# Kernel optimization log

Measured on AMD Instinct MI355X. Metric: run time of the kernel, lower is better.

## Reference

```python
import jax, jax.numpy as jnp
import numpy as np

EPS = 1e-7
NUM_HEADS = 16

def _ln(x, g, b):
    m = jnp.mean(x, -1, keepdims=True)
    v = jnp.var(x, -1, keepdims=True)
    return (x - m) * jax.lax.rsqrt(v + EPS) * g + b

def _gelu(x):
    return jax.nn.gelu(x, approximate=False)  # torch nn.GELU default = exact erf

def _attn(x, qkv_w, qkv_b, pw, pb):
    B, N, C = x.shape
    D = C // NUM_HEADS
    qkv = (x @ qkv_w.T + qkv_b).reshape(B, N, 3, NUM_HEADS, D).transpose(2, 0, 3, 1, 4)
    q, k, v = qkv[0], qkv[1], qkv[2]
    a = jax.nn.softmax(jnp.einsum('bhnd,bhmd->bhnm', q, k) * (D ** -0.5), axis=-1)
    o = jnp.einsum('bhnm,bhmd->bhnd', a, v).transpose(0, 2, 1, 3).reshape(B, N, C)
    return o @ pw.T + pb

def _gcn(x, w, b, adj):
    # x: (B,C,J); w: (C*K,C) 1x1 conv, then einsum 'nkctv,kvw->nctw' with t==1
    K = adj.shape[0]
    B, C, J = x.shape
    y = jnp.einsum('bcj,oc->boj', x, w) + b[None, :, None]
    y = y.reshape(B, K, C, J)
    return jnp.einsum('bkcv,kvw->bcw', y, adj)

def _mlp(x, w1, b1, w2, b2):
    return _gelu(_gelu(x @ w1.T + b1) @ w2.T + b2)

def _lrsc(x, adj, l1g, l1b, l2g, l2b, g1w, g1b, g2w, g2b, m1w, m1b, m2w, m2b):
    x = x.transpose(0, 2, 1)                       # (B,C,J)
    res = x
    xn = _ln(x, l1g, l1b)                          # LayerNorm over J
    x = res + _mlp(xn, m1w, m1b, m2w, m2b) + _gcn(xn, g1w, g1b, adj)
    x = _ln(x.transpose(0, 2, 1), l2g, l2b).transpose(0, 2, 1)  # LayerNorm over C
    res = x
    x = res + _mlp(x, m1w, m1b, m2w, m2b) + _gcn(x, g2w, g2b, adj)
    return x.transpose(0, 2, 1)                    # (B,J,C)

def _gkpc(x, lg, lb, q1w, q1b, p1w, p1b, q2w, q2b, p2w, p2b):
    x = x + _attn(_ln(x, lg, lb), q1w, q1b, p1w, p1b)
    return _attn(_ln(x, lg, lb), q2w, q2b, p2w, p2b)  # note: no residual on second attn

def _forward(x, adj, ln1_g, ln1_b, ln2_g, ln2_b, gcn1_w, gcn1_b, gcn2_w, gcn2_b,
             mlp1_w1, mlp1_b1, mlp1_w2, mlp1_b2, attn_ln_g, attn_ln_b,
             qkv1_w, qkv1_b, proj1_w, proj1_b, qkv2_w, qkv2_b, proj2_w, proj2_b,
             tn_g, tn_b):
    L = ln1_g.shape[0]
    for i in range(L):
        # GG_ACM/RR_ACM/LCM are published as identity -> both 0.3/0.7 mixes equal x + gelu(x)
        xin = x + _gelu(x)
        x5 = _gkpc(xin, attn_ln_g[i], attn_ln_b[i], qkv1_w[i], qkv1_b[i],
                   proj1_w[i], proj1_b[i], qkv2_w[i], qkv2_b[i], proj2_w[i], proj2_b[i])
        x7 = _lrsc(xin, adj, ln1_g[i], ln1_b[i], ln2_g[i], ln2_b[i],
                   gcn1_w[i], gcn1_b[i], gcn2_w[i], gcn2_b[i],
                   mlp1_w1[i], mlp1_b1[i], mlp1_w2[i], mlp1_b2[i])
        x = x + x5 + x7
    return _ln(x, tn_g, tn_b)

def setup_inputs():
    B, V, C, K, L = 2048, 17, 512, 3, 3
    s = 0.05
    ks = jax.random.split(jax.random.key(0), 12)
    rn = lambda k, sh: jax.random.normal(k, sh, jnp.float32) * s
    return dict(
        x=jax.random.normal(ks[0], (B, V, C), jnp.float32),
        adj=jax.random.uniform(ks[1], (K, V, V), dtype=jnp.float32),
        ln1_g=jnp.ones((L, V), jnp.float32), ln1_b=jnp.zeros((L, V), jnp.float32),
        ln2_g=jnp.ones((L, C), jnp.float32), ln2_b=jnp.zeros((L, C), jnp.float32),
        gcn1_w=rn(ks[2], (L, C * K, C)), gcn1_b=jnp.zeros((L, C * K), jnp.float32),
        gcn2_w=rn(ks[3], (L, C * K, C)), gcn2_b=jnp.zeros((L, C * K), jnp.float32),
        mlp1_w1=rn(ks[4], (L, C, V)), mlp1_b1=jnp.zeros((L, C), jnp.float32),
        mlp1_w2=rn(ks[5], (L, V, C)), mlp1_b2=jnp.zeros((L, V), jnp.float32),
        attn_ln_g=jnp.ones((L, C), jnp.float32), attn_ln_b=jnp.zeros((L, C), jnp.float32),
        qkv1_w=rn(ks[6], (L, 3 * C, C)), qkv1_b=jnp.zeros((L, 3 * C), jnp.float32),
        proj1_w=rn(ks[7], (L, C, C)), proj1_b=jnp.zeros((L, C), jnp.float32),
        qkv2_w=rn(ks[8], (L, 3 * C, C)), qkv2_b=jnp.zeros((L, 3 * C), jnp.float32),
        proj2_w=rn(ks[9], (L, C, C)), proj2_b=jnp.zeros((L, C), jnp.float32),
        tn_g=jnp.ones((C,), jnp.float32), tn_b=jnp.zeros((C,), jnp.float32),
    )

def reference(x, adj, ln1_g, ln1_b, ln2_g, ln2_b, gcn1_w, gcn1_b, gcn2_w, gcn2_b,
              mlp1_w1, mlp1_b1, mlp1_w2, mlp1_b2, attn_ln_g, attn_ln_b,
              qkv1_w, qkv1_b, proj1_w, proj1_b, qkv2_w, qkv2_b, proj2_w, proj2_b,
              tn_g, tn_b):
    return _forward(x, adj, ln1_g, ln1_b, ln2_g, ln2_b, gcn1_w, gcn1_b, gcn2_w, gcn2_b,
                    mlp1_w1, mlp1_b1, mlp1_w2, mlp1_b2, attn_ln_g, attn_ln_b,
                    qkv1_w, qkv1_b, proj1_w, proj1_b, qkv2_w, qkv2_b, proj2_w, proj2_b,
                    tn_g, tn_b)
```

## Files before the change

kernel.cpp:

```cpp
#include <hip/hip_runtime.h>
#include <hip/hip_bf16.h>
#include <math.h>

#define Bn 2048
#define Vn 17
#define Cn 512
static const size_t NE = (size_t)Bn * Vn * Cn;
#define MROWS (Bn * Vn)

typedef __attribute__((ext_vector_type(8))) short bf16x8;
typedef __attribute__((ext_vector_type(4))) float f32x4;
typedef __attribute__((ext_vector_type(2))) float f32x2;
typedef unsigned short u16;

__device__ __forceinline__ float u2f(u16 u) { return __uint_as_float(((unsigned)u) << 16); }
__device__ __forceinline__ u16 f2u(float f) {
    unsigned u = __float_as_uint(f);
    return (u16)((u + 0x7fffu + ((u >> 16) & 1u)) >> 16);
}
__device__ __forceinline__ float gelu_f(float x) {
    return 0.5f * x * (1.0f + erff(x * 0.70710678118654752f));
}
__device__ __forceinline__ float exp2f_fast(float b) {
#if __has_builtin(__builtin_amdgcn_exp2f)
    return __builtin_amdgcn_exp2f(b);
#else
    return __expf(b * 0.69314718056f);
#endif
}
__device__ __forceinline__ float gelu_fast(float x) {
    float b = x * fmaf(x * x, -0.10294348f, -2.30220820f);
    return x * __builtin_amdgcn_rcpf(1.0f + exp2f_fast(b));
}
__device__ __forceinline__ unsigned pk2(float lo, float hi) {
    __hip_bfloat162 h = __float22bfloat162_rn(make_float2(lo, hi));
    unsigned r;
    __builtin_memcpy(&r, &h, 4);
    return r;
}
__device__ __forceinline__ unsigned gelu2pk(float x0, float x1) {
    f32x2 x = {x0, x1};
    f32x2 xx = x * x;
    f32x2 t = xx * (f32x2){-0.10294348f, -0.10294348f} +
              (f32x2){-2.30220820f, -2.30220820f};
    f32x2 b = x * t;
    f32x2 e = {exp2f_fast(b[0]), exp2f_fast(b[1])};
    f32x2 d = e + (f32x2){1.0f, 1.0f};
    f32x2 r = {__builtin_amdgcn_rcpf(d[0]), __builtin_amdgcn_rcpf(d[1])};
    f32x2 g = x * r;
    return pk2(g[0], g[1]);
}
__device__ __forceinline__ void gload16(const u16* g, u16* l) {
    __builtin_amdgcn_global_load_lds((const __attribute__((address_space(1))) void*)g,
                                     (__attribute__((address_space(3))) void*)l, 16, 0, 0);
}

__global__ void k_diag(float* __restrict__ o, float v, int n) {
    int i = blockIdx.x * 256 + threadIdx.x;
    if (i < n) o[i] = v;
}

__global__ void k_f2b(const float4* __restrict__ s, ushort4* __restrict__ d, int n4) {
    int i = blockIdx.x * 256 + threadIdx.x;
    if (i >= n4) return;
    float4 v = s[i];
    ushort4 o = {f2u(v.x), f2u(v.y), f2u(v.z), f2u(v.w)};
    d[i] = o;
}

__global__ void k_mpad(const float* __restrict__ W1, const float* __restrict__ W2,
                       u16* __restrict__ W1p, u16* __restrict__ W2p) {
    int t = blockIdx.x * 256 + threadIdx.x;
    if (t < 512 * 32) {
        int o = t >> 5, j = t & 31;
        W1p[t] = (j < 17) ? f2u(W1[o * 17 + j]) : (u16)0;
    } else {
        int t2 = t - 512 * 32;
        int w = t2 >> 9;
        W2p[t2] = (w < 17) ? f2u(W2[t2]) : (u16)0;
    }
}

__global__ __launch_bounds__(256) void k_xin_lnc(const float* __restrict__ X,
                                                 const float* __restrict__ g,
                                                 const float* __restrict__ bt,
                                                 u16* __restrict__ XIN, u16* __restrict__ T,
                                                 int nrows) {
    int row = blockIdx.x * 4 + (threadIdx.x >> 6);
    if (row >= nrows) return;
    int lane = threadIdx.x & 63;
    const float* xp = X + (size_t)row * Cn + lane * 8;
    float4 v0 = *(const float4*)xp, v1 = *(const float4*)(xp + 4);
    float xv[8] = {v0.x, v0.y, v0.z, v0.w, v1.x, v1.y, v1.z, v1.w};
    bf16x8 xr;
    float vv[8];
#pragma unroll
    for (int k = 0; k < 8; k++) {
        u16 h = f2u(xv[k] + gelu_f(xv[k]));
        xr[k] = (short)h;
        vv[k] = u2f(h);
    }
    *(bf16x8*)(XIN + (size_t)row * Cn + lane * 8) = xr;
    float s = 0.f, q = 0.f;
#pragma unroll
    for (int k = 0; k < 8; k++) { s += vv[k]; q = fmaf(vv[k], vv[k], q); }
#pragma unroll
    for (int o = 32; o; o >>= 1) { s += __shfl_xor(s, o); q += __shfl_xor(q, o); }
    float mean = s * (1.f / Cn);
    float var = q * (1.f / Cn) - mean * mean;
    float inv = 1.f / sqrtf(var + 1e-7f);
    int cb = lane * 8;
    bf16x8 r;
#pragma unroll
    for (int k = 0; k < 8; k++) r[k] = f2u((vv[k] - mean) * inv * g[cb + k] + bt[cb + k]);
    *(bf16x8*)(T + (size_t)row * Cn + cb) = r;
}

template <int F32IO>
__global__ __launch_bounds__(256) void k_ln_c(const void* __restrict__ Xv,
                                              const float* __restrict__ g,
                                              const float* __restrict__ bt,
                                              void* __restrict__ Ov, int nrows) {
    int row = blockIdx.x * 4 + (threadIdx.x >> 6);
    if (row >= nrows) return;
    int lane = threadIdx.x & 63;
    float vv[8];
    if (F32IO) {
        const float* xp = (const float*)Xv + (size_t)row * Cn + lane * 8;
        float4 v0 = *(const float4*)xp, v1 = *(const float4*)(xp + 4);
        vv[0] = v0.x; vv[1] = v0.y; vv[2] = v0.z; vv[3] = v0.w;
        vv[4] = v1.x; vv[5] = v1.y; vv[6] = v1.z; vv[7] = v1.w;
    } else {
        bf16x8 h = *(const bf16x8*)((const u16*)Xv + (size_t)row * Cn + lane * 8);
#pragma unroll
        for (int k = 0; k < 8; k++) vv[k] = u2f((u16)h[k]);
    }
    float s = 0.f, q = 0.f;
#pragma unroll
    for (int k = 0; k < 8; k++) { s += vv[k]; q = fmaf(vv[k], vv[k], q); }
#pragma unroll
    for (int o = 32; o; o >>= 1) { s += __shfl_xor(s, o); q += __shfl_xor(q, o); }
    float mean = s * (1.f / Cn);
    float var = q * (1.f / Cn) - mean * mean;
    float inv = 1.f / sqrtf(var + 1e-7f);
    int cb = lane * 8;
    if (F32IO) {
        float r[8];
#pragma unroll
        for (int k = 0; k < 8; k++) r[k] = (vv[k] - mean) * inv * g[cb + k] + bt[cb + k];
        float* op = (float*)Ov + (size_t)row * Cn + cb;
        *(float4*)op = make_float4(r[0], r[1], r[2], r[3]);
        *(float4*)(op + 4) = make_float4(r[4], r[5], r[6], r[7]);
    } else {
        bf16x8 r;
#pragma unroll
        for (int k = 0; k < 8; k++) r[k] = f2u((vv[k] - mean) * inv * g[cb + k] + bt[cb + k]);
        *(bf16x8*)((u16*)Ov + (size_t)row * Cn + cb) = r;
    }
}

__global__ __launch_bounds__(256) void k_ln_j(const u16* __restrict__ X,
                                              const float* __restrict__ g,
                                              const float* __restrict__ bt,
                                              u16* __restrict__ O) {
    int idx = blockIdx.x * 256 + threadIdx.x;
    int b = idx >> 9, c = idx & 511;
    const u16* xp = X + (size_t)b * Vn * Cn + c;
    float v[Vn];
    float s = 0.f;
#pragma unroll
    for (int j = 0; j < Vn; j++) { v[j] = u2f(xp[(size_t)j * Cn]); s += v[j]; }
    float mean = s * (1.f / Vn);
    float q = 0.f;
#pragma unroll
    for (int j = 0; j < Vn; j++) { float d = v[j] - mean; q = fmaf(d, d, q); }
    float inv = 1.f / sqrtf(q * (1.f / Vn) + 1e-7f);
    u16* op = O + (size_t)b * Vn * Cn + c;
#pragma unroll
    for (int j = 0; j < Vn; j++) op[(size_t)j * Cn] = f2u((v[j] - mean) * inv * g[j] + bt[j]);
}

template <int REMAP, int EPI>
__global__ __launch_bounds__(256) void k_gemm(const u16* __restrict__ A, const u16* __restrict__ W,
                                              const float* __restrict__ bias, u16* __restrict__ OutB,
                                              const u16* __restrict__ Res, float* __restrict__ Xf,
                                              int hbase, int shift) {
    constexpr int NT = REMAP ? 6 : 8;
    const int K = 512;
    int wave = threadIdx.x >> 6, lane = threadIdx.x & 63;
    int m0 = blockIdx.x * 128 + wave * 32;
    int nbase = blockIdx.y * (16 * NT);
    int r16 = lane & 15, kq = lane >> 4;
    int ld = REMAP ? (3 << shift) : 512;

    const u16* wp[NT];
    int wrow[NT];
#pragma unroll
    for (int nt = 0; nt < NT; nt++) {
        int n = nbase + nt * 16 + r16;
        int wr;
        if (REMAP) {
            int s = n >> shift, off = n & ((1 << shift) - 1);
            wr = (s << 9) + hbase + off;
        } else wr = n;
        wrow[nt] = wr;
        wp[nt] = W + (size_t)wr * K + kq * 8;
    }
    f32x4 acc[2][NT];
#pragma unroll
    for (int i = 0; i < 2; i++)
#pragma unroll
        for (int nt = 0; nt < NT; nt++) acc[i][nt] = (f32x4){0.f, 0.f, 0.f, 0.f};

    const u16* ap = A + (size_t)(m0 + r16) * K + kq * 8;
    for (int k0 = 0; k0 < K; k0 += 32) {
        bf16x8 a0 = *(const bf16x8*)(ap + k0);
        bf16x8 a1 = *(const bf16x8*)(ap + (size_t)16 * K + k0);
#pragma unroll
        for (int nt = 0; nt < NT; nt++) {
            bf16x8 bf = *(const bf16x8*)(wp[nt] + k0);
            acc[0][nt] = __builtin_amdgcn_mfma_f32_16x16x32_bf16(a0, bf, acc[0][nt], 0, 0, 0);
            acc[1][nt] = __builtin_amdgcn_mfma_f32_16x16x32_bf16(a1, bf, acc[1][nt], 0, 0, 0);
        }
    }
#pragma unroll
    for (int nt = 0; nt < NT; nt++) {
        float bv = bias[wrow[nt]];
        int n = nbase + nt * 16 + r16;
#pragma unroll
        for (int i = 0; i < 2; i++) {
#pragma unroll
            for (int r = 0; r < 4; r++) {
                size_t mb = (size_t)(m0 + i * 16 + kq * 4 + r);
                float v = acc[i][nt][r] + bv;
                if (EPI == 0) OutB[mb * ld + n] = f2u(v);
                else if (EPI == 1) { size_t o = mb * 512 + n; OutB[o] = f2u(v + u2f(Res[o])); }
                else { size_t o = mb * 512 + n; Xf[o] += v; }
            }
        }
    }
}

template <int EPI, int NY>
__global__ __launch_bounds__(256) void k_gemm2(const u16* __restrict__ A, const u16* __restrict__ W,
                                               const float* __restrict__ bias, u16* __restrict__ OutB,
                                               const u16* __restrict__ Res, float* __restrict__ Xf,
                                               int N) {
    __shared__ u16 As[128 * 64];
    __shared__ u16 Bs[128 * 64];
    const int K = 512;
    int tid = threadIdx.x;
    int wave = tid >> 6, lane = tid & 63;
    int cpx = gridDim.x >> 3;
    int bid = blockIdx.x;
    int swz = (bid & 7) * cpx + (bid >> 3);
    int m0 = (swz / NY) * 128, n0 = (swz % NY) * 128;
    int r16 = lane & 15, kq = lane >> 4;

    int srow = wave << 2;
    int lrow = lane >> 3;
    int lcol = (lane & 7) * 8;

    f32x4 acc[2][8];
#pragma unroll
    for (int i = 0; i < 2; i++)
#pragma unroll
        for (int j = 0; j < 8; j++) acc[i][j] = (f32x4){0.f, 0.f, 0.f, 0.f};

    const u16* aT = As + (wave * 32 + r16) * 64 + kq * 8;
    const u16* bT = Bs + r16 * 64 + kq * 8;

    for (int k0 = 0; k0 < K; k0 += 64) {
#pragma unroll
        for (int i = 0; i < 4; i++) {
            int rows = (srow + i) * 8 + lrow;
            gload16(A + (size_t)(m0 + rows) * K + k0 + lcol, (u16*)As + (srow + i) * 512);
            gload16(W + (size_t)(n0 + rows) * K + k0 + lcol, (u16*)Bs + (srow + i) * 512);
        }
        __syncthreads();
#pragma unroll
        for (int kk = 0; kk < 64; kk += 32) {
            bf16x8 af0 = *(const bf16x8*)(aT + kk);
            bf16x8 af1 = *(const bf16x8*)(aT + 16 * 64 + kk);
#pragma unroll
            for (int nt = 0; nt < 8; nt++) {
                bf16x8 bf = *(const bf16x8*)(bT + nt * 16 * 64 + kk);
                acc[0][nt] = __builtin_amdgcn_mfma_f32_16x16x32_bf16(af0, bf, acc[0][nt], 0, 0, 0);
                acc[1][nt] = __builtin_amdgcn_mfma_f32_16x16x32_bf16(af1, bf, acc[1][nt], 0, 0, 0);
            }
        }
        __syncthreads();
    }

    int mw = m0 + wave * 32;
#pragma unroll
    for (int nt = 0; nt < 8; nt++) {
        int n = n0 + nt * 16 + r16;
        float bv = bias[n];
#pragma unroll
        for (int i = 0; i < 2; i++) {
#pragma unroll
            for (int r = 0; r < 4; r++) {
                size_t mb = (size_t)(mw + i * 16 + kq * 4 + r);
                size_t o = mb * N + n;
                float v = acc[i][nt][r] + bv;
                if (EPI == 0) OutB[o] = f2u(v);
                else if (EPI == 1) OutB[o] = f2u(v + u2f(Res[o]));
                else Xf[o] += v;
            }
        }
    }
}

__global__ __launch_bounds__(256) void k_attn(const u16* __restrict__ Y, u16* __restrict__ T,
                                              int shift, int hgbase, int l2ch) {
    int wv = threadIdx.x >> 6, lane = threadIdx.x & 63;
    if (lane >= 34) return;
    int gw = blockIdx.x * 4 + wv;
    int which = (lane >= 17) ? 1 : 0;
    int j = lane - which * 17;
    int pid = gw * 2 + which;
    int b = pid >> l2ch;
    int hl = pid & ((1 << l2ch) - 1);
    int CW = 1 << shift;
    int row3 = 3 << shift;

    const u16* qb = Y + (size_t)(b * Vn + j) * row3 + hl * 32;
    float q[32];
#pragma unroll
    for (int d0 = 0; d0 < 32; d0 += 8) {
        bf16x8 h = *(const bf16x8*)(qb + d0);
#pragma unroll
        for (int d = 0; d < 8; d++) q[d0 + d] = u2f((u16)h[d]);
    }
    float sc[Vn];
    float mx = -1e30f;
#pragma unroll
    for (int kk = 0; kk < Vn; kk++) {
        const u16* kb = Y + (size_t)(b * Vn + kk) * row3 + CW + hl * 32;
        float s = 0.f;
#pragma unroll
        for (int d0 = 0; d0 < 32; d0 += 8) {
            bf16x8 h = *(const bf16x8*)(kb + d0);
#pragma unroll
            for (int d = 0; d < 8; d++) s = fmaf(q[d0 + d], u2f((u16)h[d]), s);
        }
        s *= 0.1767766952966369f;
        sc[kk] = s;
        mx = fmaxf(mx, s);
    }
    float sum = 0.f;
#pragma unroll
    for (int kk = 0; kk < Vn; kk++) { sc[kk] = __expf(sc[kk] - mx); sum += sc[kk]; }
    float inv = 1.f / sum;
    float o[32];
#pragma unroll
    for (int d = 0; d < 32; d++) o[d] = 0.f;
#pragma unroll
    for (int kk = 0; kk < Vn; kk++) {
        const u16* vb = Y + (size_t)(b * Vn + kk) * row3 + 2 * CW + hl * 32;
        float p = sc[kk] * inv;
#pragma unroll
        for (int d0 = 0; d0 < 32; d0 += 8) {
            bf16x8 h = *(const bf16x8*)(vb + d0);
#pragma unroll
            for (int d = 0; d < 8; d++) o[d0 + d] = fmaf(p, u2f((u16)h[d]), o[d0 + d]);
        }
    }
    u16* op = T + (size_t)(b * Vn + j) * Cn + hgbase + hl * 32;
#pragma unroll
    for (int d0 = 0; d0 < 32; d0 += 8) {
        bf16x8 r;
#pragma unroll
        for (int d = 0; d < 8; d++) r[d] = f2u(o[d0 + d]);
        *(bf16x8*)(op + d0) = r;
    }
}

template <int MODE>
__global__ __launch_bounds__(256) void k_agg(const u16* __restrict__ Y, const float* __restrict__ Adj,
                                             const u16* __restrict__ aux1, const u16* __restrict__ aux2,
                                             u16* __restrict__ OutB, float* __restrict__ Xf,
                                             int cbase, int shift) {
    __shared__ float adj_s[3][Vn][Vn];
    for (int t = threadIdx.x; t < 3 * Vn * Vn; t += 256) {
        int k = t / (Vn * Vn), r = t - k * Vn * Vn;
        adj_s[k][r / Vn][r % Vn] = Adj[t];
    }
    __syncthreads();
    int CW = 1 << shift;
    int idx = blockIdx.x * 256 + threadIdx.x;
    int b = idx >> shift, co = idx & (CW - 1);
    int c = cbase + co;
    int row3 = 3 << shift;
    float acc[Vn];
#pragma unroll
    for (int w = 0; w < Vn; w++) acc[w] = 0.f;
    const u16* yb = Y + (size_t)b * Vn * row3 + co;
#pragma unroll
    for (int k = 0; k < 3; k++)
#pragma unroll
        for (int v = 0; v < Vn; v++) {
            float y = u2f(yb[(size_t)v * row3 + k * CW]);
#pragma unroll
            for (int w = 0; w < Vn; w++) acc[w] = fmaf(y, adj_s[k][v][w], acc[w]);
        }
    size_t rb = (size_t)(b * Vn) * Cn + c;
#pragma unroll
    for (int w = 0; w < Vn; w++) {
        size_t o = rb + (size_t)w * Cn;
        float val = acc[w] + u2f(aux1[o]) + u2f(aux2[o]);
        if (MODE == 0) OutB[o] = f2u(val);
        else Xf[o] += val;
    }
}

__global__ __launch_bounds__(512) void k_mlp(const u16* __restrict__ X,
                                             const u16* __restrict__ W1p, const float* __restrict__ B1,
                                             const u16* __restrict__ W2p, const float* __restrict__ B2,
                                             u16* __restrict__ O) {
    __shared__ u16 Xs[256 * 40];
    __shared__ u16 Hs[256 * 40];
    int b = blockIdx.x >> 1;
    int cbase = (blockIdx.x & 1) << 8;
    int tid = threadIdx.x;

    for (int i = tid; i < 256 * 40 / 8; i += 512) ((float4*)Xs)[i] = make_float4(0.f, 0.f, 0.f, 0.f);
    __syncthreads();
    const u16* xb = X + (size_t)b * (Vn * Cn) + cbase;
    for (int i = tid; i < 17 * 256; i += 512) {
        int j = i >> 8, c = i & 255;
        Xs[c * 40 + j] = xb[j * Cn + c];
    }
    __syncthreads();

    int wave = tid >> 6, lane = tid & 63;
    int r16 = lane & 15, kq = lane >> 4;
    int crow = wave * 32;

    bf16x8 xf0 = *(const bf16x8*)(Xs + (crow + r16) * 40 + kq * 8);
    bf16x8 xf1 = *(const bf16x8*)(Xs + (crow + 16 + r16) * 40 + kq * 8);

    f32x4 acc2[2][2];
#pragma unroll
    for (int i = 0; i < 2; i++)
#pragma unroll
        for (int j = 0; j < 2; j++) acc2[i][j] = (f32x4){0.f, 0.f, 0.f, 0.f};

    const u16* hs0 = Hs + (crow + r16) * 40 + kq * 8;
    const u16* w1b = W1p + (r16 << 5) + kq * 8;
    const u16* w2b = W2p + (size_t)r16 * 512 + kq * 8;
    const u16* w2c = W2p + (size_t)16 * 512 + kq * 8;
    const float* b1b = B1 + kq * 4;

#pragma unroll
    for (int s = 0; s < 16; s++) {
        bf16x8 af0 = *(const bf16x8*)(w1b + s * 1024);
        bf16x8 af1 = *(const bf16x8*)(w1b + s * 1024 + 512);
        f32x4 bi0 = *(const f32x4*)(b1b + s * 32);
        f32x4 bi1 = *(const f32x4*)(b1b + s * 32 + 16);
        f32x4 a00 = __builtin_amdgcn_mfma_f32_16x16x32_bf16(af0, xf0, bi0, 0, 0, 0);
        f32x4 a01 = __builtin_amdgcn_mfma_f32_16x16x32_bf16(af0, xf1, bi0, 0, 0, 0);
        f32x4 a10 = __builtin_amdgcn_mfma_f32_16x16x32_bf16(af1, xf0, bi1, 0, 0, 0);
        f32x4 a11 = __builtin_amdgcn_mfma_f32_16x16x32_bf16(af1, xf1, bi1, 0, 0, 0);
#define STORE_H(ACC, NT, OT)                                                             \
        {                                                                                 \
            unsigned g0 = gelu2pk(ACC[0], ACC[1]);                                        \
            unsigned g1 = gelu2pk(ACC[2], ACC[3]);                                        \
            *(uint2*)(Hs + (crow + NT * 16 + r16) * 40 + OT * 16 + kq * 4) =              \
                make_uint2(g0, g1);                                                       \
        }
        STORE_H(a00, 0, 0)
        STORE_H(a01, 1, 0)
        STORE_H(a10, 0, 1)
        STORE_H(a11, 1, 1)
#undef STORE_H
        __builtin_amdgcn_sched_barrier(0);
        bf16x8 h0 = *(const bf16x8*)hs0;
        bf16x8 h1 = *(const bf16x8*)(hs0 + 16 * 40);
        bf16x8 wf0 = *(const bf16x8*)(w2b + s * 32);
        bf16x8 wf1 = *(const bf16x8*)(w2c + s * 32);
        acc2[0][0] = __builtin_amdgcn_mfma_f32_16x16x32_bf16(h0, wf0, acc2[0][0], 0, 0, 0);
        acc2[0][1] = __builtin_amdgcn_mfma_f32_16x16x32_bf16(h0, wf1, acc2[0][1], 0, 0, 0);
        acc2[1][0] = __builtin_amdgcn_mfma_f32_16x16x32_bf16(h1, wf0, acc2[1][0], 0, 0, 0);
        acc2[1][1] = __builtin_amdgcn_mfma_f32_16x16x32_bf16(h1, wf1, acc2[1][1], 0, 0, 0);
    }

    u16* ob = O + (size_t)b * (Vn * Cn) + cbase;
#pragma unroll
    for (int nt = 0; nt < 2; nt++) {
        int cl = crow + nt * 16 + kq * 4;
#pragma unroll
        for (int n2 = 0; n2 < 2; n2++) {
            int w = n2 * 16 + r16;
            if (w < 17) {
                float bb = B2[w];
                f32x4 v = acc2[nt][n2];
                uint2 pk = make_uint2(gelu2pk(v[0] + bb, v[1] + bb),
                                      gelu2pk(v[2] + bb, v[3] + bb));
                *(uint2*)(ob + (size_t)w * Cn + cl) = pk;
            }
        }
    }
}

extern "C" void kernel_launch(void* const* d_in, const int* in_sizes, int n_in,
                              void* d_out, int out_size, void* d_ws, size_t ws_size,
                              hipStream_t stream) {
    (void)in_sizes; (void)n_in; (void)out_size;
    typedef const float* fp;
    fp x_in = (fp)d_in[0];
    fp adj = (fp)d_in[1];
    fp ln1_g = (fp)d_in[2], ln1_b = (fp)d_in[3];
    fp ln2_g = (fp)d_in[4], ln2_b = (fp)d_in[5];
    fp gcn1_w = (fp)d_in[6], gcn1_b = (fp)d_in[7];
    fp gcn2_w = (fp)d_in[8], gcn2_b = (fp)d_in[9];
    fp m1w = (fp)d_in[10], m1b = (fp)d_in[11];
    fp m2w = (fp)d_in[12], m2b = (fp)d_in[13];
    fp aln_g = (fp)d_in[14], aln_b = (fp)d_in[15];
    fp qkv1_w = (fp)d_in[16], qkv1_b = (fp)d_in[17];
    fp p1w = (fp)d_in[18], p1b = (fp)d_in[19];
    fp qkv2_w = (fp)d_in[20], qkv2_b = (fp)d_in[21];
    fp p2w = (fp)d_in[22], p2b = (fp)d_in[23];
    fp tn_g = (fp)d_in[24], tn_b = (fp)d_in[25];

    const size_t NE2 = NE * 2;
    const size_t YCH16 = (size_t)MROWS * 96 * 16 * 2;
    const size_t SZ_QKV3 = (size_t)3 * 1536 * 512;
    const size_t SZ_P3 = (size_t)3 * 512 * 512;
    const size_t MPADL = (size_t)(512 * 32 + 32 * 512);
    const size_t POOLB = (4 * SZ_QKV3 + 2 * SZ_P3 + 3 * MPADL) * 2;
    const size_t WSCR_SZ = (size_t)1536 * 512 * 2;
    const size_t MPAD_SZ = MPADL * 2;

    bool FULLW = false;
    int CH = 0;
    if (3 * NE2 + YCH16 + POOLB + 1024 <= ws_size) { FULLW = true; CH = 16; }
    else {
        for (int ch = 16; ch >= 1; ch >>= 1) {
            size_t need = 3 * NE2 + WSCR_SZ + MPAD_SZ + (size_t)MROWS * 96 * ch * 2 + 1024;
            if (need <= ws_size) { CH = ch; break; }
        }
    }
    if (!CH) {
        k_diag<<<(int)((NE + 255) / 256), 256, 0, stream>>>((float*)d_out, (float)ws_size, (int)NE);
        return;
    }
    const int l2ch = __builtin_ctz(CH);
    const int shift = 5 + l2ch;
    const int NCH = 16 / CH;
    const bool FAST = (CH == 16);

    char* p = (char*)d_ws;
    u16* XIN = (u16*)p;  p += NE2;
    u16* T1 = (u16*)p;   p += NE2;
    u16* T2 = (u16*)p;   p += NE2;
    u16* YCH = (u16*)p;  p += (size_t)MROWS * 96 * CH * 2;
    u16 *WQ1 = nullptr, *WQ2 = nullptr, *WG1 = nullptr, *WG2 = nullptr,
        *WP1 = nullptr, *WP2 = nullptr, *MP1 = nullptr, *MP2 = nullptr, *WSCR = nullptr;
    if (FULLW) {
        WQ1 = (u16*)p; p += SZ_QKV3 * 2;
        WQ2 = (u16*)p; p += SZ_QKV3 * 2;
        WG1 = (u16*)p; p += SZ_QKV3 * 2;
        WG2 = (u16*)p; p += SZ_QKV3 * 2;
        WP1 = (u16*)p; p += SZ_P3 * 2;
        WP2 = (u16*)p; p += SZ_P3 * 2;
        MP1 = (u16*)p; p += 3 * 16384 * 2;
        MP2 = (u16*)p; p += 3 * 16384 * 2;
    } else {
        WSCR = (u16*)p; p += WSCR_SZ;
        MP1 = (u16*)p;  p += 16384 * 2;
        MP2 = (u16*)p;
    }

    float* X = (float*)d_out;
    (void)hipMemcpyAsync(X, x_in, NE * 4, hipMemcpyDeviceToDevice, stream);

    if (FULLW) {
        k_f2b<<<2304, 256, 0, stream>>>((const float4*)qkv1_w, (ushort4*)WQ1, (int)(SZ_QKV3 / 4));
        k_f2b<<<2304, 256, 0, stream>>>((const float4*)qkv2_w, (ushort4*)WQ2, (int)(SZ_QKV3 / 4));
        k_f2b<<<2304, 256, 0, stream>>>((const float4*)gcn1_w, (ushort4*)WG1, (int)(SZ_QKV3 / 4));
        k_f2b<<<2304, 256, 0, stream>>>((const float4*)gcn2_w, (ushort4*)WG2, (int)(SZ_QKV3 / 4));
        k_f2b<<<768, 256, 0, stream>>>((const float4*)p1w, (ushort4*)WP1, (int)(SZ_P3 / 4));
        k_f2b<<<768, 256, 0, stream>>>((const float4*)p2w, (ushort4*)WP2, (int)(SZ_P3 / 4));
        for (int l = 0; l < 3; l++)
            k_mpad<<<128, 256, 0, stream>>>(m1w + (size_t)l * Cn * Vn, m2w + (size_t)l * Vn * Cn,
                                            MP1 + l * 16384, MP2 + l * 16384);
    }

    const int GLN = MROWS / 4;
    const int GBC = Bn * Cn / 256;
    const int GATT = (Bn << l2ch) / 8;
    const int GAGG = (Bn << shift) / 256;
    const dim3 GEMM_C(MROWS / 128, CH);
    const dim3 GEMM_P(MROWS / 128, 4);
    const int CV_QKV = (int)(1536 * 512 / 4 / 256);
    const int CV_P = (int)(512 * 512 / 4 / 256);
    const int GQF = (MROWS / 128) * 12;
    const int GPF = (MROWS / 128) * 4;

    for (int i = 0; i < 3; i++) {
        fp q1w = qkv1_w + (size_t)i * 1536 * 512, q1b = qkv1_b + i * 1536;
        fp q2w = qkv2_w + (size_t)i * 1536 * 512, q2b = qkv2_b + i * 1536;
        fp g1w = gcn1_w + (size_t)i * 1536 * 512, g1b = gcn1_b + i * 1536;
        fp g2w = gcn2_w + (size_t)i * 1536 * 512, g2b = gcn2_b + i * 1536;
        fp pw1 = p1w + (size_t)i * 512 * 512, pb1 = p1b + i * Cn;
        fp pw2 = p2w + (size_t)i * 512 * 512, pb2 = p2b + i * Cn;
        fp alg = aln_g + i * Cn, alb = aln_b + i * Cn;
        fp l1g = ln1_g + i * Vn, l1b_ = ln1_b + i * Vn;
        fp l2g = ln2_g + i * Cn, l2b_ = ln2_b + i * Cn;
        fp w1 = m1w + (size_t)i * Cn * Vn, b1 = m1b + i * Cn;
        fp w2 = m2w + (size_t)i * Vn * Cn, b2 = m2b + i * Vn;

        const u16* wq1p = FULLW ? WQ1 + (size_t)i * 1536 * 512 : WSCR;
        const u16* wq2p = FULLW ? WQ2 + (size_t)i * 1536 * 512 : WSCR;
        const u16* wg1p = FULLW ? WG1 + (size_t)i * 1536 * 512 : WSCR;
        const u16* wg2p = FULLW ? WG2 + (size_t)i * 1536 * 512 : WSCR;
        const u16* wp1p = FULLW ? WP1 + (size_t)i * 512 * 512 : WSCR;
        const u16* wp2p = FULLW ? WP2 + (size_t)i * 512 * 512 : WSCR;
        const u16* mp1 = FULLW ? MP1 + i * 16384 : MP1;
        const u16* mp2 = FULLW ? MP2 + i * 16384 : MP2;

        if (!FULLW) k_mpad<<<128, 256, 0, stream>>>(w1, w2, (u16*)mp1, (u16*)mp2);

        k_xin_lnc<<<GLN, 256, 0, stream>>>(X, alg, alb, XIN, T1, MROWS);
        if (!FULLW) k_f2b<<<CV_QKV, 256, 0, stream>>>((const float4*)q1w, (ushort4*)WSCR, 1536 * 512 / 4);
        if (FAST) {
            k_gemm2<0, 12><<<GQF, 256, 0, stream>>>(T1, wq1p, q1b, YCH, nullptr, nullptr, 1536);
            k_attn<<<GATT, 256, 0, stream>>>(YCH, T2, shift, 0, l2ch);
        } else {
            for (int hg = 0; hg < NCH; hg++) {
                k_gemm<1, 0><<<GEMM_C, 256, 0, stream>>>(T1, WSCR, q1b, YCH, nullptr, nullptr, hg << shift, shift);
                k_attn<<<GATT, 256, 0, stream>>>(YCH, T2, shift, hg << shift, l2ch);
            }
        }
        if (!FULLW) k_f2b<<<CV_P, 256, 0, stream>>>((const float4*)pw1, (ushort4*)WSCR, 512 * 512 / 4);
        if (FAST) k_gemm2<1, 4><<<GPF, 256, 0, stream>>>(T2, wp1p, pb1, T1, XIN, nullptr, 512);
        else k_gemm<0, 1><<<GEMM_P, 256, 0, stream>>>(T2, WSCR, pb1, T1, XIN, nullptr, 0, 0);
        k_ln_c<0><<<GLN, 256, 0, stream>>>(T1, alg, alb, T2, MROWS);
        if (!FULLW) k_f2b<<<CV_QKV, 256, 0, stream>>>((const float4*)q2w, (ushort4*)WSCR, 1536 * 512 / 4);
        if (FAST) {
            k_gemm2<0, 12><<<GQF, 256, 0, stream>>>(T2, wq2p, q2b, YCH, nullptr, nullptr, 1536);
            k_attn<<<GATT, 256, 0, stream>>>(YCH, T1, shift, 0, l2ch);
        } else {
            for (int hg = 0; hg < NCH; hg++) {
                k_gemm<1, 0><<<GEMM_C, 256, 0, stream>>>(T2, WSCR, q2b, YCH, nullptr, nullptr, hg << shift, shift);
                k_attn<<<GATT, 256, 0, stream>>>(YCH, T1, shift, hg << shift, l2ch);
            }
        }
        if (!FULLW) k_f2b<<<CV_P, 256, 0, stream>>>((const float4*)pw2, (ushort4*)WSCR, 512 * 512 / 4);
        if (FAST) k_gemm2<2, 4><<<GPF, 256, 0, stream>>>(T1, wp2p, pb2, nullptr, nullptr, X, 512);
        else k_gemm<0, 2><<<GEMM_P, 256, 0, stream>>>(T1, WSCR, pb2, nullptr, nullptr, X, 0, 0);

        k_ln_j<<<GBC, 256, 0, stream>>>(XIN, l1g, l1b_, T1);
        k_mlp<<<Bn * 2, 512, 0, stream>>>(T1, mp1, b1, mp2, b2, T2);
        if (!FULLW) k_f2b<<<CV_QKV, 256, 0, stream>>>((const float4*)g1w, (ushort4*)WSCR, 1536 * 512 / 4);
        if (FAST) {
            k_gemm2<0, 12><<<GQF, 256, 0, stream>>>(T1, wg1p, g1b, YCH, nullptr, nullptr, 1536);
            k_agg<0><<<GAGG, 256, 0, stream>>>(YCH, adj, XIN, T2, XIN, nullptr, 0, shift);
        } else {
            for (int cc = 0; cc < NCH; cc++) {
                k_gemm<1, 0><<<GEMM_C, 256, 0, stream>>>(T1, WSCR, g1b, YCH, nullptr, nullptr, cc << shift, shift);
                k_agg<0><<<GAGG, 256, 0, stream>>>(YCH, adj, XIN, T2, XIN, nullptr, cc << shift, shift);
            }
        }
        k_ln_c<0><<<GLN, 256, 0, stream>>>(XIN, l2g, l2b_, T1, MROWS);
        k_mlp<<<Bn * 2, 512, 0, stream>>>(T1, mp1, b1, mp2, b2, T2);
        if (!FULLW) k_f2b<<<CV_QKV, 256, 0, stream>>>((const float4*)g2w, (ushort4*)WSCR, 1536 * 512 / 4);
        if (FAST) {
            k_gemm2<0, 12><<<GQF, 256, 0, stream>>>(T1, wg2p, g2b, YCH, nullptr, nullptr, 1536);
            k_agg<1><<<GAGG, 256, 0, stream>>>(YCH, adj, T1, T2, nullptr, X, 0, shift);
        } else {
            for (int cc = 0; cc < NCH; cc++) {
                k_gemm<1, 0><<<GEMM_C, 256, 0, stream>>>(T1, WSCR, g2b, YCH, nullptr, nullptr, cc << shift, shift);
                k_agg<1><<<GAGG, 256, 0, stream>>>(YCH, adj, T1, T2, nullptr, X, cc << shift, shift);
            }
        }
    }

    k_ln_c<1><<<GLN, 256, 0, stream>>>(X, tn_g, tn_b, X, MROWS);
}
```

Measured before the change: 3.713 ms.

## Fuse QKV projection GEMM with per-head attention in one kernel

Adds a fused kernel in which each block computes the QKV projection for 119 rows (7 batches) and one head using MFMA, stages the Q/K/V tile in shared memory, and then runs the 17x17 softmax attention in place, writing the head output directly. This removes the round trip of the full 1536-wide QKV activation through global memory and one kernel launch per attention call. In exchange the GEMM tile is smaller (96 columns, 119 valid of 128 rows, so some MFMA work is wasted on clamped padding rows), and the attention phase uses only 7 of the 8 possible lane groups.

```diff
diff --git a/kernel.cpp b/kernel.cpp
--- a/kernel.cpp
+++ b/kernel.cpp
@@ -307,6 +307,135 @@
                 if (EPI == 0) OutB[o] = f2u(v);
                 else if (EPI == 1) OutB[o] = f2u(v + u2f(Res[o]));
                 else Xf[o] += v;
+            }
+        }
+    }
+}
+
+__global__ __launch_bounds__(256) void k_fat(const u16* __restrict__ A, const u16* __restrict__ W,
+                                             const float* __restrict__ bias, u16* __restrict__ T) {
+    __shared__ char smem[28672];
+    u16* As = (u16*)smem;
+    u16* Bs = (u16*)(smem + 16384);
+    u16* Ys = (u16*)smem;
+    const int K = 512;
+    int tid = threadIdx.x;
+    int wave = tid >> 6, lane = tid & 63;
+    int mb = blockIdx.x >> 4;
+    int h = blockIdx.x & 15;
+    int m0 = mb * 119;
+    int r16 = lane & 15, kq = lane >> 4;
+    int lrow = lane >> 3;
+    int lcol = (lane & 7) * 8;
+
+    f32x4 acc[2][6];
+#pragma unroll
+    for (int i = 0; i < 2; i++)
+#pragma unroll
+        for (int nt = 0; nt < 6; nt++) acc[i][nt] = (f32x4){0.f, 0.f, 0.f, 0.f};
+
+    const u16* aT = As + (wave * 32 + r16) * 64 + kq * 8;
+    const u16* bT = Bs + r16 * 64 + kq * 8;
+
+    for (int k0 = 0; k0 < K; k0 += 64) {
+#pragma unroll
+        for (int i = 0; i < 4; i++) {
+            int rows = (wave * 4 + i) * 8 + lrow;
+            int grow = m0 + rows;
+            if (grow > MROWS - 1) grow = MROWS - 1;
+            gload16(A + (size_t)grow * K + k0 + lcol, As + (wave * 4 + i) * 512);
+        }
+#pragma unroll
+        for (int i = 0; i < 3; i++) {
+            int rw = (wave * 3 + i) * 8 + lrow;
+            int wr = ((rw >> 5) << 9) + h * 32 + (rw & 31);
+            gload16(W + (size_t)wr * K + k0 + lcol, Bs + (wave * 3 + i) * 512);
+        }
+        __syncthreads();
+#pragma unroll
+        for (int kk = 0; kk < 64; kk += 32) {
+            bf16x8 af0 = *(const bf16x8*)(aT + kk);
+            bf16x8 af1 = *(const bf16x8*)(aT + 16 * 64 + kk);
+#pragma unroll
+            for (int nt = 0; nt < 6; nt++) {
+                bf16x8 bf = *(const bf16x8*)(bT + nt * 16 * 64 + kk);
+                acc[0][nt] = __builtin_amdgcn_mfma_f32_16x16x32_bf16(af0, bf, acc[0][nt], 0, 0, 0);
+                acc[1][nt] = __builtin_amdgcn_mfma_f32_16x16x32_bf16(af1, bf, acc[1][nt], 0, 0, 0);
+            }
+        }
+        __syncthreads();
+    }
+
+#pragma unroll
+    for (int nt = 0; nt < 6; nt++) {
+        int col = nt * 16 + r16;
+        int wr = ((col >> 5) << 9) + h * 32 + (col & 31);
+        float bv = bias[wr];
+#pragma unroll
+        for (int i = 0; i < 2; i++) {
+            int row = wave * 32 + i * 16 + kq * 4;
+#pragma unroll
+            for (int r = 0; r < 4; r++)
+                Ys[(row + r) * 104 + col] = f2u(acc[i][nt][r] + bv);
+        }
+    }
+    __syncthreads();
+
+    int which = (lane >= 17) ? 1 : 0;
+    int j = lane - which * 17;
+    int bl = wave * 2 + which;
+    if (lane < 34 && bl < 7) {
+        int b = mb * 7 + bl;
+        if (b < Bn) {
+            const u16* yb = Ys + (size_t)(bl * 17) * 104;
+            float q[32];
+#pragma unroll
+            for (int d0 = 0; d0 < 32; d0 += 8) {
+                bf16x8 hq = *(const bf16x8*)(yb + j * 104 + d0);
+#pragma unroll
+                for (int d = 0; d < 8; d++) q[d0 + d] = u2f((u16)hq[d]);
+            }
+            float sc[Vn];
+            float mx = -1e30f;
+#pragma unroll
+            for (int kk = 0; kk < Vn; kk++) {
+                const u16* kb = yb + kk * 104 + 32;
+                float s = 0.f;
+#pragma unroll
+                for (int d0 = 0; d0 < 32; d0 += 8) {
+                    bf16x8 hk = *(const bf16x8*)(kb + d0);
+#pragma unroll
+                    for (int d = 0; d < 8; d++) s = fmaf(q[d0 + d], u2f((u16)hk[d]), s);
+                }
+                s *= 0.1767766952966369f;
+                sc[kk] = s;
+                mx = fmaxf(mx, s);
+            }
+            float sum = 0.f;
+#pragma unroll
+            for (int kk = 0; kk < Vn; kk++) { sc[kk] = __expf(sc[kk] - mx); sum += sc[kk]; }
+            float inv = 1.f / sum;
+            float o[32];
+#pragma unroll
+            for (int d = 0; d < 32; d++) o[d] = 0.f;
+#pragma unroll
+            for (int kk = 0; kk < Vn; kk++) {
+                const u16* vb = yb + kk * 104 + 64;
+                float p = sc[kk] * inv;
+#pragma unroll
+                for (int d0 = 0; d0 < 32; d0 += 8) {
+                    bf16x8 hv = *(const bf16x8*)(vb + d0);
+#pragma unroll
+                    for (int d = 0; d < 8; d++) o[d0 + d] = fmaf(p, u2f((u16)hv[d]), o[d0 + d]);
+                }
+            }
+            u16* op = T + (size_t)(b * Vn + j) * Cn + h * 32;
+#pragma unroll
+            for (int d0 = 0; d0 < 32; d0 += 8) {
+                bf16x8 r;
+#pragma unroll
+                for (int d = 0; d < 8; d++) r[d] = f2u(o[d0 + d]);
+                *(bf16x8*)(op + d0) = r;
             }
         }
     }
@@ -598,6 +727,7 @@
     const int CV_P = (int)(512 * 512 / 4 / 256);
     const int GQF = (MROWS / 128) * 12;
     const int GPF = (MROWS / 128) * 4;
+    const int GFAT = 293 * 16;
 
     for (int i = 0; i < 3; i++) {
         fp q1w = qkv1_w + (size_t)i * 1536 * 512, q1b = qkv1_b + i * 1536;
@@ -626,8 +756,7 @@
         k_xin_lnc<<<GLN, 256, 0, stream>>>(X, alg, alb, XIN, T1, MROWS);
         if (!FULLW) k_f2b<<<CV_QKV, 256, 0, stream>>>((const float4*)q1w, (ushort4*)WSCR, 1536 * 512 / 4);
         if (FAST) {
-            k_gemm2<0, 12><<<GQF, 256, 0, stream>>>(T1, wq1p, q1b, YCH, nullptr, nullptr, 1536);
-            k_attn<<<GATT, 256, 0, stream>>>(YCH, T2, shift, 0, l2ch);
+            k_fat<<<GFAT, 256, 0, stream>>>(T1, wq1p, q1b, T2);
         } else {
             for (int hg = 0; hg < NCH; hg++) {
                 k_gemm<1, 0><<<GEMM_C, 256, 0, stream>>>(T1, WSCR, q1b, YCH, nullptr, nullptr, hg << shift, shift);
@@ -640,8 +769,7 @@
         k_ln_c<0><<<GLN, 256, 0, stream>>>(T1, alg, alb, T2, MROWS);
         if (!FULLW) k_f2b<<<CV_QKV, 256, 0, stream>>>((const float4*)q2w, (ushort4*)WSCR, 1536 * 512 / 4);
         if (FAST) {
-            k_gemm2<0, 12><<<GQF, 256, 0, stream>>>(T2, wq2p, q2b, YCH, nullptr, nullptr, 1536);
-            k_attn<<<GATT, 256, 0, stream>>>(YCH, T1, shift, 0, l2ch);
+            k_fat<<<GFAT, 256, 0, stream>>>(T2, wq2p, q2b, T1);
         } else {
             for (int hg = 0; hg < NCH; hg++) {
                 k_gemm<1, 0><<<GEMM_C, 256, 0, stream>>>(T2, WSCR, q2b, YCH, nullptr, nullptr, hg << shift, shift);
```

Result: slower. 4.194 ms (+13.0%).
